# Optimization experiments

Hardware: AMD Instinct MI355X
Metric: run time of the kernel (lower is better)

Reference implementation:

```python
import jax, jax.numpy as jnp
import numpy as np

KERNEL = 500
PAD_IDX = 256


def setup_inputs() -> dict:
    key = jax.random.key(0)
    ks = jax.random.split(key, 8)
    B, L = 8, 1_000_000
    x = jax.random.randint(ks[0], (B, L), 0, 257, dtype=jnp.int64)
    emb = jax.random.normal(ks[1], (257, 8), dtype=jnp.float32)
    emb = emb.at[PAD_IDX].set(0.0)  # padding_idx row is zero
    W1 = jax.random.normal(ks[2], (128, 8, KERNEL), dtype=jnp.float32) * 0.02
    b1 = jax.random.normal(ks[3], (128,), dtype=jnp.float32) * 0.02
    W2 = jax.random.normal(ks[4], (128, 8, KERNEL), dtype=jnp.float32) * 0.02
    b2 = jax.random.normal(ks[5], (128,), dtype=jnp.float32) * 0.02
    fcW = jax.random.normal(ks[6], (2, 128), dtype=jnp.float32) * 0.1
    fcb = jax.random.normal(ks[7], (2,), dtype=jnp.float32) * 0.1
    return {"x": x, "emb": emb, "W1": W1, "b1": b1, "W2": W2, "b2": b2, "fcW": fcW, "fcb": fcb}


def reference(x, emb, W1, b1, W2, b2, fcW, fcb):
    B, L = x.shape
    P = L // KERNEL  # non-overlapping patches (stride == kernel_size)
    # embedding with padding_idx semantics: output zero at pad positions
    e = emb[x] * (x != PAD_IDX)[..., None].astype(emb.dtype)  # [B, L, 8]
    patches = e.reshape(B, P, KERNEL, 8)                      # [B, P, K, C]
    # conv1d(k=stride=500) == patchified GEMM; weight layout [out, in, k]
    g1 = jnp.einsum('bpkc,ock->bpo', patches, W1) + b1        # [B, P, 128]
    g2 = jnp.einsum('bpkc,ock->bpo', patches, W2) + b2
    h = jax.nn.relu(g1 * jax.nn.sigmoid(g2))                  # GLU gate + relu
    m = jnp.max(h, axis=1)                                    # global max pool -> [B, 128]
    return m @ fcW.T + fcb                                    # [B, num_classes]
```

## Files before the change

### kernel.cpp

```cpp
#include <hip/hip_runtime.h>


typedef __attribute__((ext_vector_type(8))) short short8;
typedef __attribute__((ext_vector_type(4))) float f32x4;

__device__ __forceinline__ unsigned short f2b(float f) {
    union { float f; unsigned u; } un;
    un.f = f;
    unsigned u = un.u;
    return (unsigned short)((u + 0x7FFFu + ((u >> 16) & 1u)) >> 16);
}

#define KT_COUNT 125
#define WS_BBLK_BYTES (KT_COUNT * 256 * 32 * 2)
#define WS_MWS_OFF WS_BBLK_BYTES

__global__ __launch_bounds__(256) void prep_weights(
        const float* __restrict__ W1, const float* __restrict__ W2,
        unsigned short* __restrict__ Bblk, float* __restrict__ m_ws) {
    int u   = blockIdx.x * 256 + threadIdx.x;
    int kt  = u >> 10;
    int rem = u & 1023;
    int o   = rem >> 2;
    int g   = rem & 3;
    int k   = kt * 4 + g;
    const float* W = (o < 128) ? W1 : W2;
    int oo = o & 127;
    unsigned short v[8];
#pragma unroll
    for (int c = 0; c < 8; ++c) v[c] = f2b(W[oo * 4000 + c * 500 + k]);
    uint4 pack;
    pack.x = (unsigned)v[0] | ((unsigned)v[1] << 16);
    pack.y = (unsigned)v[2] | ((unsigned)v[3] << 16);
    pack.z = (unsigned)v[4] | ((unsigned)v[5] << 16);
    pack.w = (unsigned)v[6] | ((unsigned)v[7] << 16);
    *(uint4*)&Bblk[u * 8] = pack;
    if (blockIdx.x < 4) m_ws[blockIdx.x * 256 + threadIdx.x] = 0.f;
}

__global__ __launch_bounds__(512, 2) void malconv_main(
        const int* __restrict__ x, const float* __restrict__ emb,
        const float* __restrict__ b1, const float* __restrict__ b2,
        const unsigned short* __restrict__ Bblk, float* __restrict__ m_ws) {
    __shared__ __align__(16) unsigned short embb[257 * 8];

    const int t = threadIdx.x;
    for (int e = t; e < 257 * 8; e += 512) embb[e] = f2b(emb[e]);
    __syncthreads();

    const int m0   = blockIdx.x * 64;
    const int lane = t & 63, wave = t >> 6;
    const int quad = lane >> 4, l16 = lane & 15;
    const int mq   = wave >> 2, nq = wave & 3;

    const int* xp0 = x + (m0 + mq * 32 + l16) * 500 + quad;
    const int* xp1 = xp0 + 16 * 500;

    const unsigned short* bbase = Bblk + (nq * 32 + l16) * 32 + quad * 8;

    f32x4 acc[2][4];
#pragma unroll
    for (int mi = 0; mi < 2; ++mi)
#pragma unroll
        for (int ni = 0; ni < 4; ++ni) {
            f32x4 z = {0.f, 0.f, 0.f, 0.f};
            acc[mi][ni] = z;
        }

    int xc0 = xp0[0], xc1 = xp1[0];
    int xn0 = xp0[4], xn1 = xp1[4];
    short8 bcur[4];
    bcur[0] = *(const short8*)(bbase);
    bcur[1] = *(const short8*)(bbase + 512);
    bcur[2] = *(const short8*)(bbase + 4096);
    bcur[3] = *(const short8*)(bbase + 4608);

#pragma unroll 5
    for (int kt = 0; kt < KT_COUNT; ++kt) {
        int ktf = kt + 2; if (ktf > KT_COUNT - 1) ktf = KT_COUNT - 1;
        int ktb = kt + 1; if (ktb > KT_COUNT - 1) ktb = KT_COUNT - 1;
        int xf0 = xp0[ktf * 4];
        int xf1 = xp1[ktf * 4];
        const unsigned short* bb = bbase + ktb * 8192;
        short8 bnxt[4];
        bnxt[0] = *(const short8*)(bb);
        bnxt[1] = *(const short8*)(bb + 512);
        bnxt[2] = *(const short8*)(bb + 4096);
        bnxt[3] = *(const short8*)(bb + 4608);
        short8 a0 = *(const short8*)&embb[xc0 * 8];
        short8 a1 = *(const short8*)&embb[xc1 * 8];
#pragma unroll
        for (int ni = 0; ni < 4; ++ni) {
            acc[0][ni] = __builtin_amdgcn_mfma_f32_16x16x32_bf16(
                a0, bcur[ni], acc[0][ni], 0, 0, 0);
            acc[1][ni] = __builtin_amdgcn_mfma_f32_16x16x32_bf16(
                a1, bcur[ni], acc[1][ni], 0, 0, 0);
        }
        xc0 = xn0; xc1 = xn1; xn0 = xf0; xn1 = xf1;
#pragma unroll
        for (int ni = 0; ni < 4; ++ni) bcur[ni] = bnxt[ni];
    }

    const int b0 = m0 / 2000;
    const int bsplit = (b0 + 1) * 2000;
    const bool crosses = (m0 + 63) >= bsplit;
#pragma unroll
    for (int ni = 0; ni < 2; ++ni) {
        int o = nq * 32 + ni * 16 + l16;
        float bb1 = b1[o], bb2 = b2[o];
        float mx0 = 0.f, mx1 = 0.f;
#pragma unroll
        for (int mi = 0; mi < 2; ++mi)
#pragma unroll
            for (int r = 0; r < 4; ++r) {
                int ml = mq * 32 + mi * 16 + quad * 4 + r;
                float g1 = acc[mi][ni][r] + bb1;
                float g2 = acc[mi][ni + 2][r] + bb2;
                float h = fmaxf(g1 / (1.f + __expf(-g2)), 0.f);
                if (m0 + ml >= bsplit) mx1 = fmaxf(mx1, h);
                else                   mx0 = fmaxf(mx0, h);
            }
        mx0 = fmaxf(mx0, __shfl_xor(mx0, 16));
        mx0 = fmaxf(mx0, __shfl_xor(mx0, 32));
        mx1 = fmaxf(mx1, __shfl_xor(mx1, 16));
        mx1 = fmaxf(mx1, __shfl_xor(mx1, 32));
        if (quad == 0) {
            atomicMax((int*)&m_ws[b0 * 128 + o], __float_as_int(mx0));
            if (crosses)
                atomicMax((int*)&m_ws[(b0 + 1) * 128 + o], __float_as_int(mx1));
        }
    }
}

__global__ void fc_kernel(const float* __restrict__ m_ws,
                          const float* __restrict__ fcW,
                          const float* __restrict__ fcb,
                          float* __restrict__ out) {
    int t = threadIdx.x;
    if (t < 16) {
        int b = t >> 1, j = t & 1;
        float s = 0.f;
        for (int o = 0; o < 128; ++o) s += m_ws[b * 128 + o] * fcW[j * 128 + o];
        out[t] = s + fcb[j];
    }
}

extern "C" void kernel_launch(void* const* d_in, const int* in_sizes, int n_in,
                              void* d_out, int out_size, void* d_ws, size_t ws_size,
                              hipStream_t stream) {
    const int*   x   = (const int*)d_in[0];
    const float* emb = (const float*)d_in[1];
    const float* W1  = (const float*)d_in[2];
    const float* b1  = (const float*)d_in[3];
    const float* W2  = (const float*)d_in[4];
    const float* b2  = (const float*)d_in[5];
    const float* fcW = (const float*)d_in[6];
    const float* fcb = (const float*)d_in[7];
    float* out = (float*)d_out;

    unsigned short* Bblk = (unsigned short*)d_ws;
    float* m_ws = (float*)((char*)d_ws + WS_MWS_OFF);

    prep_weights<<<500, 256, 0, stream>>>(W1, W2, Bblk, m_ws);
    malconv_main<<<250, 512, 0, stream>>>(x, emb, b1, b2, Bblk, m_ws);
    fc_kernel<<<1, 64, 0, stream>>>(m_ws, fcW, fcb, out);
}
```

Baseline: 174.1 us.

## Split output channels across blocks and stage embedded A tile in LDS

The main kernel now launches 500 blocks, each owning 128 patches and one quarter of the output channels, instead of 250 blocks that each cover all channels for 64 patches. Each block cooperatively gathers the embedded A tile into double-buffered LDS, with one row per four threads, and every wave reads its 16-row fragment from there. The aim is to fill more of the device's CUs and to make the per-thread x loads coalesced. In exchange it adds a __syncthreads per k-step and reads the embedding gather four times across the channel-split blocks.

```diff
diff --git a/kernel.cpp b/kernel.cpp
--- a/kernel.cpp
+++ b/kernel.cpp
@@ -38,88 +38,89 @@
     if (blockIdx.x < 4) m_ws[blockIdx.x * 256 + threadIdx.x] = 0.f;
 }
 
-__global__ __launch_bounds__(512, 2) void malconv_main(
+__global__ __launch_bounds__(512, 4) void malconv_main(
         const int* __restrict__ x, const float* __restrict__ emb,
         const float* __restrict__ b1, const float* __restrict__ b2,
         const unsigned short* __restrict__ Bblk, float* __restrict__ m_ws) {
     __shared__ __align__(16) unsigned short embb[257 * 8];
+    __shared__ __align__(16) unsigned short Alds[2][128 * 40];
 
     const int t = threadIdx.x;
     for (int e = t; e < 257 * 8; e += 512) embb[e] = f2b(emb[e]);
+
+    const int nb = blockIdx.x & 3;
+    const int m0 = (blockIdx.x >> 2) * 128;
+    const int lane = t & 63, wave = t >> 6;
+    const int quad = lane >> 4, l16 = lane & 15;
+
+    const int ar = t >> 2, aj = t & 3;
+    const int* xptr = x + (m0 + ar) * 500 + aj;
+
+    const unsigned short* bbase = Bblk + (nb * 32 + l16) * 32 + quad * 8;
+
+    f32x4 acc[4];
+#pragma unroll
+    for (int ni = 0; ni < 4; ++ni) {
+        f32x4 z = {0.f, 0.f, 0.f, 0.f};
+        acc[ni] = z;
+    }
+
     __syncthreads();
 
-    const int m0   = blockIdx.x * 64;
-    const int lane = t & 63, wave = t >> 6;
-    const int quad = lane >> 4, l16 = lane & 15;
-    const int mq   = wave >> 2, nq = wave & 3;
-
-    const int* xp0 = x + (m0 + mq * 32 + l16) * 500 + quad;
-    const int* xp1 = xp0 + 16 * 500;
-
-    const unsigned short* bbase = Bblk + (nq * 32 + l16) * 32 + quad * 8;
-
-    f32x4 acc[2][4];
-#pragma unroll
-    for (int mi = 0; mi < 2; ++mi)
-#pragma unroll
-        for (int ni = 0; ni < 4; ++ni) {
-            f32x4 z = {0.f, 0.f, 0.f, 0.f};
-            acc[mi][ni] = z;
-        }
-
-    int xc0 = xp0[0], xc1 = xp1[0];
-    int xn0 = xp0[4], xn1 = xp1[4];
-    short8 bcur[4];
+    {
+        int xv = xptr[0];
+        *(uint4*)&Alds[0][ar * 40 + aj * 8] = *(const uint4*)&embb[xv * 8];
+    }
+    int xvn = xptr[4];
+    short8 bcur[4], bnxt[4];
     bcur[0] = *(const short8*)(bbase);
     bcur[1] = *(const short8*)(bbase + 512);
     bcur[2] = *(const short8*)(bbase + 4096);
     bcur[3] = *(const short8*)(bbase + 4608);
+    __syncthreads();
 
-#pragma unroll 5
     for (int kt = 0; kt < KT_COUNT; ++kt) {
-        int ktf = kt + 2; if (ktf > KT_COUNT - 1) ktf = KT_COUNT - 1;
-        int ktb = kt + 1; if (ktb > KT_COUNT - 1) ktb = KT_COUNT - 1;
-        int xf0 = xp0[ktf * 4];
-        int xf1 = xp1[ktf * 4];
-        const unsigned short* bb = bbase + ktb * 8192;
-        short8 bnxt[4];
-        bnxt[0] = *(const short8*)(bb);
-        bnxt[1] = *(const short8*)(bb + 512);
-        bnxt[2] = *(const short8*)(bb + 4096);
-        bnxt[3] = *(const short8*)(bb + 4608);
-        short8 a0 = *(const short8*)&embb[xc0 * 8];
-        short8 a1 = *(const short8*)&embb[xc1 * 8];
+        const int cur = kt & 1;
+        if (kt < KT_COUNT - 1) {
+            const unsigned short* bb = bbase + (kt + 1) * 8192;
+            bnxt[0] = *(const short8*)(bb);
+            bnxt[1] = *(const short8*)(bb + 512);
+            bnxt[2] = *(const short8*)(bb + 4096);
+            bnxt[3] = *(const short8*)(bb + 4608);
+        }
+        short8 afrag = *(const short8*)
+            &Alds[cur][(wave * 16 + l16) * 40 + quad * 8];
+        if (kt < KT_COUNT - 1) {
+            *(uint4*)&Alds[cur ^ 1][ar * 40 + aj * 8] =
+                *(const uint4*)&embb[xvn * 8];
+            if (kt < KT_COUNT - 2) xvn = xptr[(kt + 2) * 4];
+        }
 #pragma unroll
-        for (int ni = 0; ni < 4; ++ni) {
-            acc[0][ni] = __builtin_amdgcn_mfma_f32_16x16x32_bf16(
-                a0, bcur[ni], acc[0][ni], 0, 0, 0);
-            acc[1][ni] = __builtin_amdgcn_mfma_f32_16x16x32_bf16(
-                a1, bcur[ni], acc[1][ni], 0, 0, 0);
-        }
-        xc0 = xn0; xc1 = xn1; xn0 = xf0; xn1 = xf1;
+        for (int ni = 0; ni < 4; ++ni)
+            acc[ni] = __builtin_amdgcn_mfma_f32_16x16x32_bf16(
+                afrag, bcur[ni], acc[ni], 0, 0, 0);
 #pragma unroll
         for (int ni = 0; ni < 4; ++ni) bcur[ni] = bnxt[ni];
+        __syncthreads();
     }
 
     const int b0 = m0 / 2000;
     const int bsplit = (b0 + 1) * 2000;
-    const bool crosses = (m0 + 63) >= bsplit;
+    const bool crosses = (m0 + 127) >= bsplit && bsplit <= 16000 - 1;
 #pragma unroll
     for (int ni = 0; ni < 2; ++ni) {
-        int o = nq * 32 + ni * 16 + l16;
+        int o = nb * 32 + ni * 16 + l16;
         float bb1 = b1[o], bb2 = b2[o];
         float mx0 = 0.f, mx1 = 0.f;
 #pragma unroll
-        for (int mi = 0; mi < 2; ++mi)
-#pragma unroll
-            for (int r = 0; r < 4; ++r) {
-                int ml = mq * 32 + mi * 16 + quad * 4 + r;
-                float g1 = acc[mi][ni][r] + bb1;
-                float g2 = acc[mi][ni + 2][r] + bb2;
-                float h = fmaxf(g1 / (1.f + __expf(-g2)), 0.f);
-                if (m0 + ml >= bsplit) mx1 = fmaxf(mx1, h);
-                else                   mx0 = fmaxf(mx0, h);
-            }
+        for (int r = 0; r < 4; ++r) {
+            int ml = wave * 16 + quad * 4 + r;
+            float g1 = acc[ni][r] + bb1;
+            float g2 = acc[ni + 2][r] + bb2;
+            float h = fmaxf(g1 / (1.f + __expf(-g2)), 0.f);
+            if (m0 + ml >= bsplit) mx1 = fmaxf(mx1, h);
+            else                   mx0 = fmaxf(mx0, h);
+        }
         mx0 = fmaxf(mx0, __shfl_xor(mx0, 16));
         mx0 = fmaxf(mx0, __shfl_xor(mx0, 32));
         mx1 = fmaxf(mx1, __shfl_xor(mx1, 16));
@@ -162,6 +163,6 @@
     float* m_ws = (float*)((char*)d_ws + WS_MWS_OFF);
 
     prep_weights<<<500, 256, 0, stream>>>(W1, W2, Bblk, m_ws);
-    malconv_main<<<250, 512, 0, stream>>>(x, emb, b1, b2, Bblk, m_ws);
+    malconv_main<<<500, 512, 0, stream>>>(x, emb, b1, b2, Bblk, m_ws);
     fc_kernel<<<1, 64, 0, stream>>>(m_ws, fcW, fcb, out);
 }
```

Result: slower. 204.5 us (+17.4%).
